# Kernel tuning notes

Hardware: AMD Instinct MI355X
Metric: run time of the kernel (lower is better)

## Reference

```python
import jax, jax.numpy as jnp
import numpy as np

THRESH = 0.6


def _build_targets(targets, anchors, nH, nW, nA):
    # Vectorized replacement of the torch per-target python double loop.
    B, T, _ = targets.shape
    valid = jnp.sum(targets, axis=-1) != 0            # [B,T] skip all-zero rows
    label = targets[..., 0].astype(jnp.int32)
    gx = targets[..., 1] * nW
    gy = targets[..., 2] * nH
    gw = targets[..., 3] * nW
    gh = targets[..., 4] * nH
    gi = jnp.floor(gx).astype(jnp.int32)              # int(gx)
    gj = jnp.floor(gy).astype(jnp.int32)              # int(gy)
    aw, ah = anchors[:, 0], anchors[:, 1]             # [A]
    # IoU of (0,0,gw,gh) vs (0,0,aw,ah): co-centered boxes
    inter = jnp.minimum(gw[..., None], aw) * jnp.minimum(gh[..., None], ah)
    union = gw[..., None] * gh[..., None] + aw * ah - inter
    iou = inter / union                               # [B,T,A]
    best = jnp.argmax(iou, axis=-1)                   # [B,T]
    b_idx = jnp.broadcast_to(jnp.arange(B)[:, None], (B, T))
    safe_b = jnp.where(valid, b_idx, B)               # OOB batch idx -> scatter dropped
    a_all = jnp.broadcast_to(jnp.arange(nA), (B, T, nA))
    hb = jnp.where(valid[..., None] & (iou > THRESH), b_idx[..., None], B)

    Z = lambda: jnp.zeros((B, nA, nH, nW), jnp.float32)
    conf_mask = jnp.ones((B, nA, nH, nW), jnp.float32)
    conf_mask = conf_mask.at[hb, a_all, gj[..., None], gi[..., None]].set(0.0)
    conf_mask = conf_mask.at[safe_b, best, gj, gi].set(1.0)
    mask = Z().at[safe_b, best, gj, gi].set(1.0)
    tx = Z().at[safe_b, best, gj, gi].set(gx - jnp.floor(gx))
    ty = Z().at[safe_b, best, gj, gi].set(gy - jnp.floor(gy))
    tw = Z().at[safe_b, best, gj, gi].set(jnp.log(gw / aw[best] + 1e-16))
    th = Z().at[safe_b, best, gj, gi].set(jnp.log(gh / ah[best] + 1e-16))
    tlabel = jnp.zeros((B, nA, nH, nW), jnp.int32).at[safe_b, best, gj, gi].set(label)
    return mask, conf_mask, tx, ty, tw, th, tlabel


def reference(x, targets, anchors):
    B = x.shape[0]
    nA = anchors.shape[0]
    nH, nW = x.shape[2], x.shape[3]
    attrs = x.shape[1] // nA                          # 7 + num_classes
    pred = x.reshape(B, nA, attrs, nH, nW).transpose(0, 1, 3, 4, 2)  # [B,A,H,W,attrs]
    px = jax.nn.sigmoid(pred[..., 0])
    py = jax.nn.sigmoid(pred[..., 1])
    pw = pred[..., 2]
    ph = pred[..., 3]
    pconf = jax.nn.sigmoid(pred[..., 6])
    pcls = jax.nn.sigmoid(pred[..., 7:])              # [B,A,H,W,C]

    mask, conf_mask, tx, ty, tw, th, tlabel = _build_targets(targets, anchors, nH, nW, nA)

    n_obj = jnp.sum(mask)
    mmean = lambda d: jnp.sum(d * mask) / n_obj       # masked MSE (size_average)
    loss_x = mmean((px - tx) ** 2)
    loss_y = mmean((py - ty) ** 2)
    loss_w = mmean((pw - tw) ** 2)
    loss_h = mmean((ph - th) ** 2)

    tconf = mask
    p = jnp.clip(pconf, 1e-7, 1.0 - 1e-7)
    bce_el = -(tconf * jnp.log(p) + (1.0 - tconf) * jnp.log1p(-p))
    noobj = conf_mask * (1.0 - mask)                  # conf_mask - mask (byte sub)
    loss_conf = jnp.sum(bce_el * noobj) / jnp.sum(noobj) + jnp.sum(bce_el * mask) / n_obj

    # CrossEntropy on sigmoided class scores (faithful to the torch quirk)
    logp = jax.nn.log_softmax(pcls, axis=-1)
    ce = -jnp.take_along_axis(logp, tlabel[..., None], axis=-1)[..., 0]
    loss_cls = (1.0 / B) * jnp.sum(ce * mask) / n_obj

    return loss_x + loss_y + loss_w + loss_h + loss_conf + loss_cls


def setup_inputs() -> dict:
    key = jax.random.key(0)
    k1, k2, k3 = jax.random.split(key, 3)
    B, nA, nC, nH, nW, T = 8, 5, 8, 192, 192, 50
    x = jax.random.normal(k1, (B, nA * (7 + nC), nH, nW), jnp.float32)
    # targets: (label, cx, cy, w, h); coords normalized in (0,1)
    coords = jax.random.uniform(k2, (B, T, 4), jnp.float32, 1e-3, 0.999)
    labels = jax.random.randint(k3, (B, T, 1), 0, nC).astype(jnp.float32)
    targets = jnp.concatenate([labels, coords], axis=-1)
    anchors = jnp.array([[1.08, 1.19], [3.42, 4.41], [6.63, 11.38],
                         [9.42, 5.11], [16.62, 10.52]], jnp.float32)
    return {"x": x, "targets": targets, "anchors": anchors}
```

## Files before the change

kernel.cpp:

```cpp
#include <hip/hip_runtime.h>
#include <math.h>

#define BB 8
#define NA 5
#define NC 8
#define NH 192
#define NW 192
#define TT 50
#define ATTRS 15
#define THRESH_F 0.6f

#define NTGT (BB * TT)
static const size_t FLAGS_N = (size_t)BB * NA * NH * NW;
#define ACC_OFF  FLAGS_N
#define NACC 8
#define PART_OFF (ACC_OFF + NACC * sizeof(double))
#define CONF_BLOCKS 1440

struct Rec {
    int cell;
    int label;
    float tx, ty, tw, th;
    int valid;
    int pad;
};

__device__ __forceinline__ float sigmoidf_(float v) {
    return 1.0f / (1.0f + expf(-v));
}

__global__ __launch_bounds__(512) void build_obj_k(const float* __restrict__ x,
                                                   const float* __restrict__ tgt,
                                                   const float* __restrict__ anchors,
                                                   unsigned int* __restrict__ flags_w,
                                                   double* __restrict__ acc) {
    __shared__ Rec srecs[NTGT];
    __shared__ double wsum[8][8];
    const int tid = threadIdx.x;

    if (tid < NTGT) {
        const int b = tid / TT;
        const float* p = tgt + (size_t)tid * 5;
        float lab = p[0], cx = p[1], cy = p[2], cw = p[3], ch = p[4];
        int valid = ((lab + cx + cy + cw + ch) != 0.0f) ? 1 : 0;
        float gx = cx * NW, gy = cy * NH, gw = cw * NW, gh = ch * NH;
        int gi = min(max((int)floorf(gx), 0), NW - 1);
        int gj = min(max((int)floorf(gy), 0), NH - 1);
        float ious[NA];
        float aw[NA], ah[NA];
        int best = 0; float bi = -1.0f;
        #pragma unroll
        for (int a = 0; a < NA; ++a) {
            aw[a] = anchors[2 * a];
            ah[a] = anchors[2 * a + 1];
            float inter = fminf(gw, aw[a]) * fminf(gh, ah[a]);
            float un = gw * gh + aw[a] * ah[a] - inter;
            float iou = inter / un;
            ious[a] = iou;
            if (iou > bi) { bi = iou; best = a; }
        }
        if (valid) {
            #pragma unroll
            for (int a = 0; a < NA; ++a) {
                if (ious[a] > THRESH_F) {
                    size_t fi = (((size_t)b * NA + a) * NH + gj) * NW + gi;
                    atomicOr(&flags_w[fi >> 2], 1u << ((fi & 3) * 8));
                }
            }
            size_t fb = (((size_t)b * NA + best) * NH + gj) * NW + gi;
            atomicOr(&flags_w[fb >> 2], 2u << ((fb & 3) * 8));
        }
        Rec r;
        r.valid = valid;
        r.cell = (best * NH + gj) * NW + gi;
        r.label = (int)lab;
        r.tx = gx - floorf(gx);
        r.ty = gy - floorf(gy);
        r.tw = logf(gw / aw[best] + 1e-16f);
        r.th = logf(gh / ah[best] + 1e-16f);
        srecs[tid] = r;
    }
    __syncthreads();

    double v[7];
    #pragma unroll
    for (int k = 0; k < 7; ++k) v[k] = 0.0;

    if (tid < NTGT) {
        Rec r = srecs[tid];
        if (r.valid) {
            const int b = tid / TT, t = tid % TT;
            bool superseded = false;
            for (int t2 = t + 1; t2 < TT; ++t2) {
                Rec r2 = srecs[b * TT + t2];
                if (r2.valid && r2.cell == r.cell) { superseded = true; break; }
            }
            if (!superseded) {
                const size_t CH = (size_t)NH * NW;
                int a  = r.cell / (NH * NW);
                int hw = r.cell % (NH * NW);
                size_t base = ((size_t)(b * NA + a) * ATTRS) * CH + hw;
                float v0 = x[base + 0 * CH];
                float v1 = x[base + 1 * CH];
                float v2 = x[base + 2 * CH];
                float v3 = x[base + 3 * CH];
                float v6 = x[base + 6 * CH];
                float px = sigmoidf_(v0);
                float py = sigmoidf_(v1);
                float pconf = fminf(fmaxf(sigmoidf_(v6), 1e-7f), 1.0f - 1e-7f);
                float c[NC];
                float m = -INFINITY;
                #pragma unroll
                for (int k = 0; k < NC; ++k) {
                    float sv = sigmoidf_(x[base + (size_t)(7 + k) * CH]);
                    c[k] = sv;
                    m = fmaxf(m, sv);
                }
                float se = 0.0f;
                #pragma unroll
                for (int k = 0; k < NC; ++k) se += expf(c[k] - m);
                float lse = m + logf(se);
                v[0] = 1.0;
                v[1] = (double)((px - r.tx) * (px - r.tx));
                v[2] = (double)((py - r.ty) * (py - r.ty));
                v[3] = (double)((v2 - r.tw) * (v2 - r.tw));
                v[4] = (double)((v3 - r.th) * (v3 - r.th));
                v[5] = (double)(-logf(pconf));
                v[6] = (double)(lse - c[r.label]);
            }
        }
    }

    #pragma unroll
    for (int k = 0; k < 7; ++k)
        for (int off = 32; off > 0; off >>= 1)
            v[k] += __shfl_down(v[k], off);
    const int lane = tid & 63, wid = tid >> 6;
    if (lane == 0) {
        #pragma unroll
        for (int k = 0; k < 7; ++k) wsum[wid][k] = v[k];
    }
    __syncthreads();
    if (tid == 0) {
        #pragma unroll
        for (int k = 0; k < 7; ++k) {
            double s = 0.0;
            #pragma unroll
            for (int w = 0; w < 8; ++w) s += wsum[w][k];
            acc[k] = s;
        }
    }
}

__global__ __launch_bounds__(256) void conf_pass_k(const float* __restrict__ x,
                                                   const unsigned char* __restrict__ flags,
                                                   double* __restrict__ partials) {
    __shared__ double wsum[4][2];
    const size_t CH = (size_t)NH * NW;
    const int N4 = (BB * NA * NH * NW) / 4;
    double s_bce = 0.0;
    float s_cnt = 0.0f;
    for (int n4 = blockIdx.x * blockDim.x + threadIdx.x; n4 < N4;
         n4 += gridDim.x * blockDim.x) {
        int n = n4 * 4;
        int b = n / (NA * NH * NW);
        int rr = n % (NA * NH * NW);
        int a = rr / (NH * NW);
        int hw = rr % (NH * NW);
        size_t xi = ((size_t)(b * NA + a) * ATTRS + 6) * CH + hw;
        float4 v = *reinterpret_cast<const float4*>(x + xi);
        uchar4 f = *reinterpret_cast<const uchar4*>(flags + n);
        float vv[4] = {v.x, v.y, v.z, v.w};
        unsigned char ff[4] = {f.x, f.y, f.z, f.w};
        #pragma unroll
        for (int e = 0; e < 4; ++e) {
            if (ff[e]) continue;
            float p = fminf(fmaxf(sigmoidf_(vv[e]), 1e-7f), 1.0f - 1e-7f);
            s_bce += (double)(-log1pf(-p));
            s_cnt += 1.0f;
        }
    }
    double s_cd = (double)s_cnt;
    for (int off = 32; off > 0; off >>= 1) {
        s_bce += __shfl_down(s_bce, off);
        s_cd  += __shfl_down(s_cd, off);
    }
    const int lane = threadIdx.x & 63, wid = threadIdx.x >> 6;
    if (lane == 0) { wsum[wid][0] = s_bce; wsum[wid][1] = s_cd; }
    __syncthreads();
    if (threadIdx.x == 0) {
        double b0 = 0.0, c0 = 0.0;
        #pragma unroll
        for (int w = 0; w < 4; ++w) { b0 += wsum[w][0]; c0 += wsum[w][1]; }
        partials[2 * blockIdx.x]     = b0;
        partials[2 * blockIdx.x + 1] = c0;
    }
}

__global__ __launch_bounds__(256) void finalize_k(const double* __restrict__ acc,
                                                  const double* __restrict__ partials,
                                                  float* __restrict__ out) {
    __shared__ double wsum[4][2];
    double sb = 0.0, sc = 0.0;
    for (int i = threadIdx.x; i < CONF_BLOCKS; i += 256) {
        sb += partials[2 * i];
        sc += partials[2 * i + 1];
    }
    for (int off = 32; off > 0; off >>= 1) {
        sb += __shfl_down(sb, off);
        sc += __shfl_down(sc, off);
    }
    const int lane = threadIdx.x & 63, wid = threadIdx.x >> 6;
    if (lane == 0) { wsum[wid][0] = sb; wsum[wid][1] = sc; }
    __syncthreads();
    if (threadIdx.x == 0) {
        double b0 = 0.0, c0 = 0.0;
        #pragma unroll
        for (int w = 0; w < 4; ++w) { b0 += wsum[w][0]; c0 += wsum[w][1]; }
        double n_obj = acc[0];
        double loss = (acc[1] + acc[2] + acc[3] + acc[4]) / n_obj
                    + b0 / c0
                    + acc[5] / n_obj
                    + (1.0 / (double)BB) * acc[6] / n_obj;
        out[0] = (float)loss;
    }
}

extern "C" void kernel_launch(void* const* d_in, const int* in_sizes, int n_in,
                              void* d_out, int out_size, void* d_ws, size_t ws_size,
                              hipStream_t stream) {
    const float* x       = (const float*)d_in[0];
    const float* tgt     = (const float*)d_in[1];
    const float* anchors = (const float*)d_in[2];

    unsigned int* flags_w = (unsigned int*)d_ws;
    unsigned char* flags  = (unsigned char*)d_ws;
    double* acc      = (double*)((char*)d_ws + ACC_OFF);
    double* partials = (double*)((char*)d_ws + PART_OFF);

    hipMemsetAsync(d_ws, 0, FLAGS_N, stream);

    build_obj_k<<<1, 512, 0, stream>>>(x, tgt, anchors, flags_w, acc);
    conf_pass_k<<<CONF_BLOCKS, 256, 0, stream>>>(x, flags, partials);
    finalize_k<<<1, 256, 0, stream>>>(acc, partials, (float*)d_out);
}
```

Before: 146.0 us.

## Replace dense flag buffer with shared hash set and subtract flagged cells

```diff
diff --git a/kernel.cpp b/kernel.cpp
--- a/kernel.cpp
+++ b/kernel.cpp
@@ -11,11 +11,17 @@
 #define THRESH_F 0.6f
 
 #define NTGT (BB * TT)
-static const size_t FLAGS_N = (size_t)BB * NA * NH * NW;
-#define ACC_OFF  FLAGS_N
-#define NACC 8
-#define PART_OFF (ACC_OFF + NACC * sizeof(double))
-#define CONF_BLOCKS 1440
+#define PLANE (NH * NW)
+#define BATCH_CELLS (NA * PLANE)
+#define NCELLS (BB * BATCH_CELLS)
+#define HSZ 4096
+#define HEMPTY 0xFFFFFFFFu
+
+#define TICK_OFF 128
+#define PART_OFF 192
+#define CONF_BLOCKS 360
+#define CONF_THREADS 256
+#define CONF_TOTAL (CONF_BLOCKS * CONF_THREADS)
 
 struct Rec {
     int cell;
@@ -29,14 +35,26 @@
     return 1.0f / (1.0f + expf(-v));
 }
 
+__device__ __forceinline__ float noobj_term(float v) {
+    float p = fminf(fmaxf(sigmoidf_(v), 1e-7f), 1.0f - 1e-7f);
+    return -log1pf(-p);
+}
+
 __global__ __launch_bounds__(512) void build_obj_k(const float* __restrict__ x,
                                                    const float* __restrict__ tgt,
                                                    const float* __restrict__ anchors,
-                                                   unsigned int* __restrict__ flags_w,
-                                                   double* __restrict__ acc) {
+                                                   double* __restrict__ acc,
+                                                   unsigned int* __restrict__ ticket) {
     __shared__ Rec srecs[NTGT];
-    __shared__ double wsum[8][8];
+    __shared__ unsigned int hset[HSZ];
+    __shared__ double wsum[8][9];
     const int tid = threadIdx.x;
+
+    for (int i = tid; i < HSZ; i += 512) hset[i] = HEMPTY;
+    if (tid == 0) *ticket = 0u;
+    __syncthreads();
+
+    double corr_b = 0.0, corr_c = 0.0;
 
     if (tid < NTGT) {
         const int b = tid / TT;
@@ -61,14 +79,29 @@
         }
         if (valid) {
             #pragma unroll
-            for (int a = 0; a < NA; ++a) {
-                if (ious[a] > THRESH_F) {
-                    size_t fi = (((size_t)b * NA + a) * NH + gj) * NW + gi;
-                    atomicOr(&flags_w[fi >> 2], 1u << ((fi & 3) * 8));
+            for (int a = 0; a <= NA; ++a) {
+                int aa; bool doit;
+                if (a < NA) { aa = a; doit = (ious[a] > THRESH_F); }
+                else        { aa = best; doit = true; }
+                if (!doit) continue;
+                unsigned int key = (unsigned int)((b * NA + aa) * PLANE + gj * NW + gi);
+                unsigned int h = (key * 2654435761u) & (HSZ - 1);
+                while (true) {
+                    unsigned int old = atomicCAS(&hset[h], HEMPTY, key);
+                    if (old == HEMPTY) {
+                        int cb = key / BATCH_CELLS;
+                        int cr = key % BATCH_CELLS;
+                        int ca = cr / PLANE;
+                        int chw = cr % PLANE;
+                        float v = x[((size_t)(cb * NA + ca) * ATTRS + 6) * PLANE + chw];
+                        corr_b += (double)noobj_term(v);
+                        corr_c += 1.0;
+                        break;
+                    }
+                    if (old == key) break;
+                    h = (h + 1) & (HSZ - 1);
                 }
             }
-            size_t fb = (((size_t)b * NA + best) * NH + gj) * NW + gi;
-            atomicOr(&flags_w[fb >> 2], 2u << ((fb & 3) * 8));
         }
         Rec r;
         r.valid = valid;
@@ -82,9 +115,11 @@
     }
     __syncthreads();
 
-    double v[7];
+    double v[9];
     #pragma unroll
-    for (int k = 0; k < 7; ++k) v[k] = 0.0;
+    for (int k = 0; k < 9; ++k) v[k] = 0.0;
+    v[7] = corr_b;
+    v[8] = corr_c;
 
     if (tid < NTGT) {
         Rec r = srecs[tid];
@@ -96,15 +131,14 @@
                 if (r2.valid && r2.cell == r.cell) { superseded = true; break; }
             }
             if (!superseded) {
-                const size_t CH = (size_t)NH * NW;
-                int a  = r.cell / (NH * NW);
-                int hw = r.cell % (NH * NW);
-                size_t base = ((size_t)(b * NA + a) * ATTRS) * CH + hw;
-                float v0 = x[base + 0 * CH];
-                float v1 = x[base + 1 * CH];
-                float v2 = x[base + 2 * CH];
-                float v3 = x[base + 3 * CH];
-                float v6 = x[base + 6 * CH];
+                int a  = r.cell / PLANE;
+                int hw = r.cell % PLANE;
+                size_t base = ((size_t)(b * NA + a) * ATTRS) * PLANE + hw;
+                float v0 = x[base + 0 * PLANE];
+                float v1 = x[base + 1 * PLANE];
+                float v2 = x[base + 2 * PLANE];
+                float v3 = x[base + 3 * PLANE];
+                float v6 = x[base + 6 * PLANE];
                 float px = sigmoidf_(v0);
                 float py = sigmoidf_(v1);
                 float pconf = fminf(fmaxf(sigmoidf_(v6), 1e-7f), 1.0f - 1e-7f);
@@ -112,7 +146,7 @@
                 float m = -INFINITY;
                 #pragma unroll
                 for (int k = 0; k < NC; ++k) {
-                    float sv = sigmoidf_(x[base + (size_t)(7 + k) * CH]);
+                    float sv = sigmoidf_(x[base + (size_t)(7 + k) * PLANE]);
                     c[k] = sv;
                     m = fmaxf(m, sv);
                 }
@@ -132,18 +166,18 @@
     }
 
     #pragma unroll
-    for (int k = 0; k < 7; ++k)
+    for (int k = 0; k < 9; ++k)
         for (int off = 32; off > 0; off >>= 1)
             v[k] += __shfl_down(v[k], off);
     const int lane = tid & 63, wid = tid >> 6;
     if (lane == 0) {
         #pragma unroll
-        for (int k = 0; k < 7; ++k) wsum[wid][k] = v[k];
+        for (int k = 0; k < 9; ++k) wsum[wid][k] = v[k];
     }
     __syncthreads();
     if (tid == 0) {
         #pragma unroll
-        for (int k = 0; k < 7; ++k) {
+        for (int k = 0; k < 9; ++k) {
             double s = 0.0;
             #pragma unroll
             for (int w = 0; w < 8; ++w) s += wsum[w][k];
@@ -152,74 +186,54 @@
     }
 }
 
-__global__ __launch_bounds__(256) void conf_pass_k(const float* __restrict__ x,
-                                                   const unsigned char* __restrict__ flags,
-                                                   double* __restrict__ partials) {
-    __shared__ double wsum[4][2];
-    const size_t CH = (size_t)NH * NW;
-    const int N4 = (BB * NA * NH * NW) / 4;
-    double s_bce = 0.0;
-    float s_cnt = 0.0f;
-    for (int n4 = blockIdx.x * blockDim.x + threadIdx.x; n4 < N4;
-         n4 += gridDim.x * blockDim.x) {
+__global__ __launch_bounds__(256) void conf_fused_k(const float* __restrict__ x,
+                                                    const double* __restrict__ acc,
+                                                    unsigned int* __restrict__ ticket,
+                                                    double* __restrict__ partials,
+                                                    float* __restrict__ out) {
+    __shared__ double wred[4];
+    __shared__ int s_last;
+    const int g = blockIdx.x * CONF_THREADS + threadIdx.x;
+    double s = 0.0;
+    #pragma unroll
+    for (int it = 0; it < 4; ++it) {
+        int n4 = g + it * CONF_TOTAL;
         int n = n4 * 4;
-        int b = n / (NA * NH * NW);
-        int rr = n % (NA * NH * NW);
-        int a = rr / (NH * NW);
-        int hw = rr % (NH * NW);
-        size_t xi = ((size_t)(b * NA + a) * ATTRS + 6) * CH + hw;
-        float4 v = *reinterpret_cast<const float4*>(x + xi);
-        uchar4 f = *reinterpret_cast<const uchar4*>(flags + n);
-        float vv[4] = {v.x, v.y, v.z, v.w};
-        unsigned char ff[4] = {f.x, f.y, f.z, f.w};
-        #pragma unroll
-        for (int e = 0; e < 4; ++e) {
-            if (ff[e]) continue;
-            float p = fminf(fmaxf(sigmoidf_(vv[e]), 1e-7f), 1.0f - 1e-7f);
-            s_bce += (double)(-log1pf(-p));
-            s_cnt += 1.0f;
-        }
-    }
-    double s_cd = (double)s_cnt;
-    for (int off = 32; off > 0; off >>= 1) {
-        s_bce += __shfl_down(s_bce, off);
-        s_cd  += __shfl_down(s_cd, off);
-    }
+        int b = n / BATCH_CELLS;
+        int rr = n % BATCH_CELLS;
+        int a = rr / PLANE;
+        int hw = rr % PLANE;
+        const float4 v = *reinterpret_cast<const float4*>(
+            x + ((size_t)(b * NA + a) * ATTRS + 6) * PLANE + hw);
+        s += (double)noobj_term(v.x) + (double)noobj_term(v.y)
+           + (double)noobj_term(v.z) + (double)noobj_term(v.w);
+    }
+    for (int off = 32; off > 0; off >>= 1) s += __shfl_down(s, off);
     const int lane = threadIdx.x & 63, wid = threadIdx.x >> 6;
-    if (lane == 0) { wsum[wid][0] = s_bce; wsum[wid][1] = s_cd; }
+    if (lane == 0) wred[wid] = s;
     __syncthreads();
     if (threadIdx.x == 0) {
-        double b0 = 0.0, c0 = 0.0;
-        #pragma unroll
-        for (int w = 0; w < 4; ++w) { b0 += wsum[w][0]; c0 += wsum[w][1]; }
-        partials[2 * blockIdx.x]     = b0;
-        partials[2 * blockIdx.x + 1] = c0;
-    }
-}
-
-__global__ __launch_bounds__(256) void finalize_k(const double* __restrict__ acc,
-                                                  const double* __restrict__ partials,
-                                                  float* __restrict__ out) {
-    __shared__ double wsum[4][2];
-    double sb = 0.0, sc = 0.0;
-    for (int i = threadIdx.x; i < CONF_BLOCKS; i += 256) {
-        sb += partials[2 * i];
-        sc += partials[2 * i + 1];
-    }
-    for (int off = 32; off > 0; off >>= 1) {
-        sb += __shfl_down(sb, off);
-        sc += __shfl_down(sc, off);
-    }
-    const int lane = threadIdx.x & 63, wid = threadIdx.x >> 6;
-    if (lane == 0) { wsum[wid][0] = sb; wsum[wid][1] = sc; }
+        partials[blockIdx.x] = wred[0] + wred[1] + wred[2] + wred[3];
+        __threadfence();
+        unsigned int t = atomicAdd(ticket, 1u);
+        s_last = (t == CONF_BLOCKS - 1) ? 1 : 0;
+    }
+    __syncthreads();
+    if (!s_last) return;
+
+    __threadfence();
+    double sb = 0.0;
+    for (int i = threadIdx.x; i < CONF_BLOCKS; i += CONF_THREADS) sb += partials[i];
+    for (int off = 32; off > 0; off >>= 1) sb += __shfl_down(sb, off);
+    if (lane == 0) wred[wid] = sb;
     __syncthreads();
     if (threadIdx.x == 0) {
-        double b0 = 0.0, c0 = 0.0;
-        #pragma unroll
-        for (int w = 0; w < 4; ++w) { b0 += wsum[w][0]; c0 += wsum[w][1]; }
+        double dense = wred[0] + wred[1] + wred[2] + wred[3];
         double n_obj = acc[0];
+        double noobj_b = dense - acc[7];
+        double noobj_c = (double)NCELLS - acc[8];
         double loss = (acc[1] + acc[2] + acc[3] + acc[4]) / n_obj
-                    + b0 / c0
+                    + noobj_b / noobj_c
                     + acc[5] / n_obj
                     + (1.0 / (double)BB) * acc[6] / n_obj;
         out[0] = (float)loss;
@@ -233,14 +247,11 @@
     const float* tgt     = (const float*)d_in[1];
     const float* anchors = (const float*)d_in[2];
 
-    unsigned int* flags_w = (unsigned int*)d_ws;
-    unsigned char* flags  = (unsigned char*)d_ws;
-    double* acc      = (double*)((char*)d_ws + ACC_OFF);
-    double* partials = (double*)((char*)d_ws + PART_OFF);
-
-    hipMemsetAsync(d_ws, 0, FLAGS_N, stream);
-
-    build_obj_k<<<1, 512, 0, stream>>>(x, tgt, anchors, flags_w, acc);
-    conf_pass_k<<<CONF_BLOCKS, 256, 0, stream>>>(x, flags, partials);
-    finalize_k<<<1, 256, 0, stream>>>(acc, partials, (float*)d_out);
-}
+    double* acc          = (double*)d_ws;
+    unsigned int* ticket = (unsigned int*)((char*)d_ws + TICK_OFF);
+    double* partials     = (double*)((char*)d_ws + PART_OFF);
+
+    build_obj_k<<<1, 512, 0, stream>>>(x, tgt, anchors, acc, ticket);
+    conf_fused_k<<<CONF_BLOCKS, CONF_THREADS, 0, stream>>>(x, acc, ticket, partials,
+                                                           (float*)d_out);
+}
```

Measured after the change: 154.7 us. +5.9%, slower.
